# Kernel tuning notes

Hardware: AMD Instinct MI355X
Metric: run time of the kernel (lower is better)

The kernel has to match this reference:

```python
import jax, jax.numpy as jnp
import numpy as np

B, S, D, H, HID = 4, 1024, 1024, 16, 4096
DK = D // H
EPS = 1e-6


def _ln(x):
    # LayerNorm without affine, eps=1e-6
    mu = jnp.mean(x, axis=-1, keepdims=True)
    var = jnp.var(x, axis=-1, keepdims=True)
    return (x - mu) / jnp.sqrt(var + EPS)


def _lin(x, W, b):
    # torch Linear convention: W is [out, in]
    y = jnp.einsum('...i,oi->...o', x, W)
    return y + b if b is not None else y


def setup_inputs() -> dict:
    key = jax.random.key(0)
    ks = jax.random.split(key, 16)
    sc = lambda fan_in: 1.0 / np.sqrt(fan_in)
    inp = {
        'x': jax.random.normal(ks[0], (B, S, D), jnp.float32),
        'cond': jax.random.normal(ks[1], (B, 1, D), jnp.float32),
        'Wq': jax.random.normal(ks[2], (D, D), jnp.float32) * sc(D),
        'bq': jnp.zeros((D,), jnp.float32),
        'Wk': jax.random.normal(ks[3], (D, D), jnp.float32) * sc(D),
        'bk': jnp.zeros((D,), jnp.float32),
        'Wv': jax.random.normal(ks[4], (D, D), jnp.float32) * sc(D),
        'bv': jnp.zeros((D,), jnp.float32),
        'Wo': jax.random.normal(ks[5], (D, D), jnp.float32) * sc(D),
        'bo': jnp.zeros((D,), jnp.float32),
        'W1': jax.random.normal(ks[6], (HID, D), jnp.float32) * sc(D),
        'b1': jnp.zeros((HID,), jnp.float32),
        'W2': jax.random.normal(ks[7], (D, HID), jnp.float32) * sc(HID),
        'b2': jnp.zeros((D,), jnp.float32),
        'Wada': jax.random.normal(ks[8], (6 * D, D), jnp.float32) * sc(D),
        'bada': jnp.zeros((6 * D,), jnp.float32),
    }
    return inp


def reference(x, cond, Wq, bq, Wk, bk, Wv, bv, Wo, bo, W1, b1, W2, b2, Wada, bada):
    # adaLN modulation: SiLU -> Linear -> chunk 6 along last dim
    mod = _lin(jax.nn.silu(cond), Wada, bada)  # [B,1,6D]
    gama1, beta1, alpha1, gama2, beta2, alpha2 = jnp.split(mod, 6, axis=-1)

    # attention branch
    residual = x
    h = _ln(x) * (1.0 + beta1) + gama1  # modulate(shift=gama1, scale=beta1)
    q = _lin(h, Wq, bq).reshape(B, S, H, DK)
    k = _lin(h, Wk, bk).reshape(B, S, H, DK)
    v = _lin(h, Wv, bv).reshape(B, S, H, DK)
    scores = jnp.einsum('bqhd,bkhd->bhqk', q, k) / jnp.sqrt(jnp.float32(DK))
    probs = jax.nn.softmax(scores, axis=-1)
    attn = jnp.einsum('bhqk,bkhd->bqhd', probs, v).reshape(B, S, D)
    attn = _lin(attn, Wo, bo)
    x = residual + alpha1 * attn

    # MLP branch
    residual = x
    h = _ln(x) * (1.0 + beta2) + gama2
    h = _lin(h, W1, b1)
    h = jax.nn.gelu(h, approximate=False)  # torch nn.GELU default (erf)
    h = _lin(h, W2, b2)
    return residual + alpha2 * h
```

## Files before the change

### kernel.cpp

```cpp
#include <hip/hip_runtime.h>
#include <cstdint>

typedef __bf16 bf16_t;
typedef __bf16 bf16x4 __attribute__((ext_vector_type(4)));
typedef __bf16 bf16x8 __attribute__((ext_vector_type(8)));
typedef float f32x4 __attribute__((ext_vector_type(4)));

#define B_ 4
#define S_ 1024
#define D_ 1024
#define HID_ 4096
#define MEG (1u << 20)

static const size_t OFF_WBF  = 0;
static const size_t OFF_BQKV = 25165824;
static const size_t OFF_MOD  = 25178112;
static const size_t OFF_H    = 25276416;
static const size_t OFF_QKV  = 33665024;
static const size_t OFF_VT   = 58830848;
static const size_t OFF_ATTN = 67219456;
static const size_t OFF_X1   = 75608064;
static const size_t OFF_PART = 92385280;
static const size_t OFF_MLPH = 159494144;

__device__ __forceinline__ void async_copy16(const bf16_t* g, bf16_t* l) {
  __builtin_amdgcn_global_load_lds(
      (__attribute__((address_space(1))) void*)(g),
      (__attribute__((address_space(3))) void*)(l), 16, 0, 0);
}

__global__ __launch_bounds__(256) void convert_pack(
    const float* __restrict__ Wq, const float* __restrict__ Wk,
    const float* __restrict__ Wv, const float* __restrict__ Wo,
    const float* __restrict__ W1, const float* __restrict__ W2,
    const float* __restrict__ bq, const float* __restrict__ bk,
    const float* __restrict__ bv, bf16_t* __restrict__ wbf,
    float* __restrict__ bqkv) {
  const int y = blockIdx.y;
  if (y == 6) {
    int i = blockIdx.x * 256 + threadIdx.x;
    if (i < 3072)
      bqkv[i] = i < 1024 ? bq[i] : (i < 2048 ? bk[i - 1024] : bv[i - 2048]);
    return;
  }
  const float* src; bf16_t* dst; int n;
  switch (y) {
    case 0: src = Wq; dst = wbf;           n = MEG;     break;
    case 1: src = Wk; dst = wbf + MEG;     n = MEG;     break;
    case 2: src = Wv; dst = wbf + 2*MEG;   n = MEG;     break;
    case 3: src = Wo; dst = wbf + 3*MEG;   n = MEG;     break;
    case 4: src = W1; dst = wbf + 4*MEG;   n = 4*MEG;   break;
    default: src = W2; dst = wbf + 8*MEG;  n = 4*MEG;   break;
  }
  int idx = (blockIdx.x * 256 + threadIdx.x) * 4;
  if (idx < n) {
    float4 v = *(const float4*)(src + idx);
    bf16x4 pk;
    pk.x = (__bf16)v.x; pk.y = (__bf16)v.y; pk.z = (__bf16)v.z; pk.w = (__bf16)v.w;
    *(bf16x4*)(dst + idx) = pk;
  }
}

__global__ __launch_bounds__(256) void ada_mod(
    const float* __restrict__ cond, const float* __restrict__ Wada,
    const float* __restrict__ bada, float* __restrict__ mod) {
  const int wave = threadIdx.x >> 6, lane = threadIdx.x & 63;
  const int o = blockIdx.x * 4 + wave;
  const float* wr = Wada + (size_t)o * D_;
  float a0 = 0.f, a1 = 0.f, a2 = 0.f, a3 = 0.f;
#pragma unroll
  for (int l = 0; l < 16; l++) {
    int i = l * 64 + lane;
    float w = wr[i];
    float c0 = cond[i], c1 = cond[1024 + i], c2 = cond[2048 + i], c3 = cond[3072 + i];
    a0 += w * (c0 / (1.0f + __expf(-c0)));
    a1 += w * (c1 / (1.0f + __expf(-c1)));
    a2 += w * (c2 / (1.0f + __expf(-c2)));
    a3 += w * (c3 / (1.0f + __expf(-c3)));
  }
#pragma unroll
  for (int offs = 32; offs; offs >>= 1) {
    a0 += __shfl_xor(a0, offs);
    a1 += __shfl_xor(a1, offs);
    a2 += __shfl_xor(a2, offs);
    a3 += __shfl_xor(a3, offs);
  }
  if (lane == 0) {
    float bb = bada[o];
    mod[o]          = a0 + bb;
    mod[6144 + o]   = a1 + bb;
    mod[12288 + o]  = a2 + bb;
    mod[18432 + o]  = a3 + bb;
  }
}

__global__ __launch_bounds__(256) void ln_modulate(
    const float* __restrict__ X, const float* __restrict__ mod,
    bf16_t* __restrict__ H, int goff) {
  const int row = blockIdx.x;
  const int b = row >> 10;
  const int t = threadIdx.x;
  const float* xr = X + (size_t)row * D_;
  float4 xv = *(const float4*)(xr + t * 4);
  float s = xv.x + xv.y + xv.z + xv.w;
  float q = xv.x*xv.x + xv.y*xv.y + xv.z*xv.z + xv.w*xv.w;
  const int wave = t >> 6, lane = t & 63;
#pragma unroll
  for (int offs = 32; offs; offs >>= 1) {
    s += __shfl_down(s, offs);
    q += __shfl_down(q, offs);
  }
  __shared__ float sb[4][2];
  if (lane == 0) { sb[wave][0] = s; sb[wave][1] = q; }
  __syncthreads();
  float st = sb[0][0] + sb[1][0] + sb[2][0] + sb[3][0];
  float qt = sb[0][1] + sb[1][1] + sb[2][1] + sb[3][1];
  float mu = st * (1.0f / D_);
  float var = qt * (1.0f / D_) - mu * mu;
  float rstd = rsqrtf(var + 1e-6f);
  const float* mb = mod + (size_t)b * 6144 + goff;
  const int c = t * 4;
  float4 gm = *(const float4*)(mb + c);
  float4 bt = *(const float4*)(mb + 1024 + c);
  bf16x4 pk;
  pk.x = (__bf16)((xv.x - mu) * rstd * (1.0f + bt.x) + gm.x);
  pk.y = (__bf16)((xv.y - mu) * rstd * (1.0f + bt.y) + gm.y);
  pk.z = (__bf16)((xv.z - mu) * rstd * (1.0f + bt.z) + gm.z);
  pk.w = (__bf16)((xv.w - mu) * rstd * (1.0f + bt.w) + gm.w);
  *(bf16x4*)(H + (size_t)row * D_ + c) = pk;
}

__global__ __launch_bounds__(256) void transpose_v(
    const bf16_t* __restrict__ qkv, bf16_t* __restrict__ vT) {
  __shared__ bf16_t tile[64][65];
  const int bh = blockIdx.y;
  const int b = bh >> 4, hh = bh & 15;
  const int s0 = blockIdx.x * 64;
  const int t = threadIdx.x;
  const int tx = t & 63, ty = t >> 6;
  const bf16_t* src = qkv + (size_t)b * S_ * 3072 + 2048 + hh * 64;
  for (int r = ty; r < 64; r += 4)
    tile[r][tx] = src[(size_t)(s0 + r) * 3072 + tx];
  __syncthreads();
  bf16_t* dst = vT + (size_t)bh * 64 * 1024;
  for (int r = ty; r < 64; r += 4)
    dst[(size_t)r * 1024 + s0 + tx] = tile[tx][r];
}

__global__ __launch_bounds__(512, 4) void flash_attn(
    const bf16_t* __restrict__ qkv, const bf16_t* __restrict__ vT,
    bf16_t* __restrict__ attn) {
  __shared__ __align__(16) bf16_t Ks[2][2][64 * 64];
  __shared__ __align__(16) bf16_t Vs[2][2][64 * 64];
  __shared__ __align__(16) bf16_t Ps[8][16 * 64];

  const int t = threadIdx.x;
  const int wave = t >> 6, lane = t & 63;
  const int lm = lane & 15, quad = lane >> 4;
  const int bh = blockIdx.y;
  const int b = bh >> 4, hh = bh & 15;
  const int s0 = blockIdx.x * 128;

  const bf16_t* qbase = qkv + (size_t)b * S_ * 3072 + hh * 64;
  const bf16_t* kbase = qbase + 1024;
  const bf16_t* vbase = vT + (size_t)bh * (64 * 1024);

  const int row0 = t >> 3;
  const int cg = (t & 7) ^ (row0 & 7);
  const int od = t * 8;

  async_copy16(qbase + (size_t)(s0 + row0) * 3072 + cg * 8, &Ks[1][0][od]);
  async_copy16(qbase + (size_t)(s0 + 64 + row0) * 3072 + cg * 8, &Ks[1][1][od]);
  async_copy16(kbase + (size_t)row0 * 3072 + cg * 8, &Ks[0][0][od]);
  async_copy16(kbase + (size_t)(64 + row0) * 3072 + cg * 8, &Ks[0][1][od]);
  async_copy16(vbase + (size_t)row0 * 1024 + cg * 8, &Vs[0][0][od]);
  async_copy16(vbase + (size_t)row0 * 1024 + 64 + cg * 8, &Vs[0][1][od]);
  __syncthreads();

  bf16x8 aq0, aq1;
  {
    const int rq = wave * 16 + lm;
    const int qh = rq >> 6, qr = rq & 63;
    const int rbq = lm & 7;
    aq0 = *(const bf16x8*)&Ks[1][qh][qr * 64 + (quad ^ rbq) * 8];
    aq1 = *(const bf16x8*)&Ks[1][qh][qr * 64 + ((4 + quad) ^ rbq) * 8];
  }
  __syncthreads();

  f32x4 accO[4] = {};
  float mrow[4], lsum[4];
#pragma unroll
  for (int r = 0; r < 4; r++) { mrow[r] = -1e30f; lsum[r] = 0.f; }

  const float SC = 0.18033688f;
  const int rb = lm & 7;
  bf16_t* Pw = Ps[wave];

  for (int tt = 0; tt < 8; ++tt) {
    const int cur = tt & 1;
    if (tt < 7) {
      const int nb = cur ^ 1;
      const size_t k0n = (size_t)(tt + 1) << 7;
      async_copy16(kbase + (k0n + row0) * 3072 + cg * 8, &Ks[nb][0][od]);
      async_copy16(kbase + (k0n + 64 + row0) * 3072 + cg * 8, &Ks[nb][1][od]);
      async_copy16(vbase + (size_t)row0 * 1024 + k0n + cg * 8, &Vs[nb][0][od]);
      async_copy16(vbase + (size_t)row0 * 1024 + k0n + 64 + cg * 8, &Vs[nb][1][od]);
    }

    f32x4 accS[8];
#pragma unroll
    for (int j = 0; j < 8; j++) accS[j] = (f32x4){0.f, 0.f, 0.f, 0.f};
    __builtin_amdgcn_s_setprio(1);
#pragma unroll
    for (int hf = 0; hf < 2; hf++) {
#pragma unroll
      for (int ni = 0; ni < 4; ni++) {
        const int rk = ni * 16 + lm;
        bf16x8 b0 = *(const bf16x8*)&Ks[cur][hf][rk * 64 + ((quad ^ rb)) * 8];
        bf16x8 b1 = *(const bf16x8*)&Ks[cur][hf][rk * 64 + (((4 + quad) ^ rb)) * 8];
        f32x4 a = accS[hf * 4 + ni];
        a = __builtin_amdgcn_mfma_f32_16x16x32_bf16(aq0, b0, a, 0, 0, 0);
        a = __builtin_amdgcn_mfma_f32_16x16x32_bf16(aq1, b1, a, 0, 0, 0);
        accS[hf * 4 + ni] = a;
      }
    }
    __builtin_amdgcn_s_setprio(0);

    float mx[4];
#pragma unroll
    for (int r = 0; r < 4; r++) {
      float m0 = fmaxf(fmaxf(accS[0][r], accS[1][r]), fmaxf(accS[2][r], accS[3][r]));
      float m1 = fmaxf(fmaxf(accS[4][r], accS[5][r]), fmaxf(accS[6][r], accS[7][r]));
      float m8 = fmaxf(m0, m1);
      m8 = fmaxf(m8, __shfl_xor(m8, 1));
      m8 = fmaxf(m8, __shfl_xor(m8, 2));
      m8 = fmaxf(m8, __shfl_xor(m8, 4));
      m8 = fmaxf(m8, __shfl_xor(m8, 8));
      mx[r] = m8 * SC;
    }
    bool ok = (mx[0] - mrow[0] <= 8.0f) && (mx[1] - mrow[1] <= 8.0f) &&
              (mx[2] - mrow[2] <= 8.0f) && (mx[3] - mrow[3] <= 8.0f);
    if (!__all(ok)) {
#pragma unroll
      for (int r = 0; r < 4; r++) {
        float mnew = fmaxf(mrow[r], mx[r]);
        float al = exp2f(mrow[r] - mnew);
        mrow[r] = mnew;
        lsum[r] *= al;
#pragma unroll
        for (int di = 0; di < 4; di++) accO[di][r] *= al;
      }
    }
#pragma unroll
    for (int r = 0; r < 4; r++) {
      float sum = 0.f;
#pragma unroll
      for (int j = 0; j < 8; j++) {
        float p = exp2f(accS[j][r] * SC - mrow[r]);
        accS[j][r] = p;
        sum += p;
      }
      lsum[r] += sum;
    }

#pragma unroll
    for (int hf = 0; hf < 2; hf++) {
#pragma unroll
      for (int jj = 0; jj < 4; jj++)
#pragma unroll
        for (int r = 0; r < 4; r++) {
          int prow = quad * 4 + r;
          int c = jj * 16 + lm;
          Pw[prow * 64 + (((c >> 3) ^ (prow & 7)) << 3) + (c & 7)] =
              (__bf16)accS[hf * 4 + jj][r];
        }
      __builtin_amdgcn_s_setprio(1);
#pragma unroll
      for (int loc = 0; loc < 2; loc++) {
        bf16x8 ap = *(const bf16x8*)&Pw[lm * 64 + (((loc * 4 + quad) ^ rb)) * 8];
#pragma unroll
        for (int di = 0; di < 4; di++) {
          const int rv = di * 16 + lm;
          bf16x8 vv = *(const bf16x8*)&Vs[cur][hf]
              [rv * 64 + (((loc * 4 + quad) ^ rb)) * 8];
          accO[di] = __builtin_amdgcn_mfma_f32_16x16x32_bf16(ap, vv, accO[di], 0, 0, 0);
        }
      }
      __builtin_amdgcn_s_setprio(0);
    }
    __syncthreads();
  }

#pragma unroll
  for (int r = 0; r < 4; r++) {
    float sv = lsum[r];
    sv += __shfl_xor(sv, 1);
    sv += __shfl_xor(sv, 2);
    sv += __shfl_xor(sv, 4);
    sv += __shfl_xor(sv, 8);
    lsum[r] = sv;
  }

#pragma unroll
  for (int r = 0; r < 4; r++) {
    float inv = 1.0f / lsum[r];
    int prow = quad * 4 + r;
#pragma unroll
    for (int di = 0; di < 4; di++) {
      int col = di * 16 + lm;
      int cph = (col >> 3) ^ (prow & 7);
      Pw[prow * 64 + cph * 8 + (col & 7)] = (__bf16)(accO[di][r] * inv);
    }
  }
  bf16_t* abase = attn + (size_t)b * S_ * 1024 +
                  (size_t)(s0 + wave * 16) * 1024 + hh * 64;
#pragma unroll
  for (int it = 0; it < 2; it++) {
    int slot = it * 64 + lane;
    int orow = slot >> 3;
    int gc = slot & 7;
    int cph = gc ^ (orow & 7);
    bf16x8 val = *(const bf16x8*)&Pw[orow * 64 + cph * 8];
    *(bf16x8*)(abase + (size_t)orow * 1024 + gc * 8) = val;
  }
}

template <int EPI>
__global__ __launch_bounds__(512) void gemm_bt_big(
    const bf16_t* __restrict__ A, int lda,
    const bf16_t* __restrict__ B, int ldb,
    bf16_t* __restrict__ C, int ldc,
    int M, int N, int K,
    const float* __restrict__ bias) {
  __shared__ __align__(16) bf16_t As[2][4][64 * 64];
  __shared__ __align__(16) bf16_t Bs[2][4][64 * 64];

  const int gx = gridDim.x;
  int d = blockIdx.x + gx * blockIdx.y;
  const int cpx = (gx * gridDim.y) >> 3;
  int wg = (d & 7) * cpx + (d >> 3);
  const int by = wg / gx;
  const int bx = wg % gx;

  const int t = threadIdx.x;
  const int wave = t >> 6;
  const int lane = t & 63;
  const int lm = lane & 15;
  const int quad = lane >> 4;
  const int wr = wave >> 2;
  const int wc = wave & 3;

  const int m0 = by * 256;
  const int n0 = bx * 256;

  f32x4 acc[8][4] = {};

  const int srow = t >> 3;
  const int scg = (t & 7) ^ (srow & 7);
  const int sod = t * 8;
  const bf16_t* Ag = A + (size_t)(m0 + srow) * lda + scg * 8;
  const bf16_t* Bg = B + (size_t)(n0 + srow) * ldb + scg * 8;
  const size_t aStep = (size_t)64 * lda;
  const size_t bStep = (size_t)64 * ldb;

#define STAGE8(buf, ko)                                        \
  async_copy16(Ag + (ko), &As[buf][0][sod]);                   \
  async_copy16(Ag + aStep + (ko), &As[buf][1][sod]);           \
  async_copy16(Ag + 2 * aStep + (ko), &As[buf][2][sod]);       \
  async_copy16(Ag + 3 * aStep + (ko), &As[buf][3][sod]);       \
  async_copy16(Bg + (ko), &Bs[buf][0][sod]);                   \
  async_copy16(Bg + bStep + (ko), &Bs[buf][1][sod]);           \
  async_copy16(Bg + 2 * bStep + (ko), &Bs[buf][2][sod]);       \
  async_copy16(Bg + 3 * bStep + (ko), &Bs[buf][3][sod]);

  const int niter = K >> 6;
  STAGE8(0, 0);
  STAGE8(1, 64);

  const int rbx = lm & 7;
  const int sl0 = (quad ^ rbx) * 8;
  const int sl1 = ((4 + quad) ^ rbx) * 8;
  const int abase = wr * 8192 + lm * 64;
  const int bbase = wc * 4096 + lm * 64;

  int cur = 0;
  for (int it = 0; it < niter; ++it) {
    if (it + 1 < niter) {
      asm volatile("s_waitcnt vmcnt(8)" ::: "memory");
    } else {
      asm volatile("s_waitcnt vmcnt(0)" ::: "memory");
    }
    __builtin_amdgcn_s_barrier();

    const bf16_t* Ac = &As[cur][0][0];
    const bf16_t* Bc = &Bs[cur][0][0];

    bf16x8 afr[8][2], bfr[4][2];
#pragma unroll
    for (int mi = 0; mi < 8; mi++) {
      const int aoff = abase + (mi >> 2) * 4096 + (mi & 3) * 1024;
      afr[mi][0] = *(const bf16x8*)&Ac[aoff + sl0];
      afr[mi][1] = *(const bf16x8*)&Ac[aoff + sl1];
    }
#pragma unroll
    for (int ni = 0; ni < 4; ni++) {
      bfr[ni][0] = *(const bf16x8*)&Bc[bbase + ni * 1024 + sl0];
      bfr[ni][1] = *(const bf16x8*)&Bc[bbase + ni * 1024 + sl1];
    }
    asm volatile("s_waitcnt lgkmcnt(0)" ::: "memory");
    __builtin_amdgcn_sched_barrier(0);
    __builtin_amdgcn_s_barrier();

    if (it + 2 < niter) {
      const int ko = (it + 2) << 6;
      STAGE8(cur, ko);
    }

    __builtin_amdgcn_s_setprio(1);
#pragma unroll
    for (int mi = 0; mi < 8; mi++)
#pragma unroll
      for (int ni = 0; ni < 4; ni++) {
        acc[mi][ni] = __builtin_amdgcn_mfma_f32_16x16x32_bf16(
            afr[mi][0], bfr[ni][0], acc[mi][ni], 0, 0, 0);
        acc[mi][ni] = __builtin_amdgcn_mfma_f32_16x16x32_bf16(
            afr[mi][1], bfr[ni][1], acc[mi][ni], 0, 0, 0);
      }
    __builtin_amdgcn_s_setprio(0);
    cur ^= 1;
  }
#undef STAGE8

#pragma unroll
  for (int mi = 0; mi < 8; mi++) {
#pragma unroll
    for (int ni = 0; ni < 4; ni++) {
#pragma unroll
      for (int r = 0; r < 4; r++) {
        int row = m0 + wr * 128 + mi * 16 + quad * 4 + r;
        int col = n0 + wc * 64 + ni * 16 + lm;
        float v = acc[mi][ni][r];
        size_t idx = (size_t)row * ldc + col;
        if (EPI == 0) {
          if (bias) v += bias[col];
          C[idx] = (__bf16)v;
        } else if (EPI == 3) {
          v += bias[col];
          float u = 1.5957691216f * (v + 0.044715f * v * v * v);
          float g = v / (1.0f + __expf(-u));
          C[idx] = (__bf16)g;
        }
      }
    }
  }
}

template <int EPI>
__global__ __launch_bounds__(512) void gemm_bt(
    const bf16_t* __restrict__ A, int lda, long long sAz,
    const bf16_t* __restrict__ B, int ldb, long long sBz,
    void* __restrict__ Cv, int ldc, long long sCz,
    int M, int N, int K,
    const float* __restrict__ bias,
    float scale) {
  __shared__ __align__(16) bf16_t As[3][256 * 64];
  __shared__ __align__(16) bf16_t Bs[3][128 * 64];

  const int z = blockIdx.z;
  A += (size_t)z * sAz;
  B += (size_t)z * sBz;

  const int gx = gridDim.x;
  int d = blockIdx.x + gx * blockIdx.y;
  {
    const int cpx = (gx * gridDim.y) >> 3;
    int wg = (d & 7) * cpx + (d >> 3);
    const int by = wg / gx;
    const int bx = wg % gx;

    const int t = threadIdx.x;
    const int wave = t >> 6;
    const int lane = t & 63;
    const int lm = lane & 15;
    const int quad = lane >> 4;
    const int wr = wave >> 1;
    const int wc = wave & 1;

    const int m0 = by * 256;
    const int n0 = bx * 128;

    f32x4 acc[4][4] = {};

    const int srow = t >> 3;
    const int scg = (t & 7) ^ (srow & 7);
    const int sod = t * 8;
    const bf16_t* Ag = A + (size_t)(m0 + srow) * lda + scg * 8;
    const bf16_t* Bg = B + (size_t)(n0 + srow) * ldb + scg * 8;
    const size_t a64 = (size_t)64 * lda, a128 = (size_t)128 * lda,
                 a192 = (size_t)192 * lda, b64 = (size_t)64 * ldb;

#define STAGE6(buf, ko)                                      \
  async_copy16(Ag + (ko), &As[buf][sod]);                    \
  async_copy16(Ag + a64 + (ko), &As[buf][4096 + sod]);       \
  async_copy16(Ag + a128 + (ko), &As[buf][8192 + sod]);      \
  async_copy16(Ag + a192 + (ko), &As[buf][12288 + sod]);     \
  async_copy16(Bg + (ko), &Bs[buf][sod]);                    \
  async_copy16(Bg + b64 + (ko), &Bs[buf][4096 + sod]);

    const int niter = K >> 6;
    STAGE6(0, 0);
    STAGE6(1, 64);

    const int rbx = lm & 7;
    const int sl0 = (quad ^ rbx) * 8;
    const int sl1 = ((4 + quad) ^ rbx) * 8;
    const int arow = wr * 4096 + lm * 64;
    const int brow = wc * 4096 + lm * 64;

    int cur = 0;
    for (int it = 0; it < niter; ++it) {
      if (it + 1 < niter) {
        asm volatile("s_waitcnt vmcnt(6)" ::: "memory");
      } else {
        asm volatile("s_waitcnt vmcnt(0)" ::: "memory");
      }
      __builtin_amdgcn_s_barrier();
      const int nb = (cur >= 1) ? cur - 1 : 2;
      const int ko = (it + 2) << 6;
      const bool st = (it + 2 < niter);

      bf16x8 af0[2], af1[2], bfr[4][2];
      af0[0] = *(const bf16x8*)&As[cur][arow + sl0];
      af0[1] = *(const bf16x8*)&As[cur][arow + sl1];
      af1[0] = *(const bf16x8*)&As[cur][arow + 1024 + sl0];
      af1[1] = *(const bf16x8*)&As[cur][arow + 1024 + sl1];
#pragma unroll
      for (int i = 0; i < 4; i++) {
        bfr[i][0] = *(const bf16x8*)&Bs[cur][brow + i * 1024 + sl0];
        bfr[i][1] = *(const bf16x8*)&Bs[cur][brow + i * 1024 + sl1];
      }
      if (st) {
        async_copy16(Ag + ko, &As[nb][sod]);
        async_copy16(Ag + a64 + ko, &As[nb][4096 + sod]);
        async_copy16(Ag + a128 + ko, &As[nb][8192 + sod]);
      }
      __builtin_amdgcn_s_barrier();
      __builtin_amdgcn_s_setprio(1);
#pragma unroll
      for (int ks = 0; ks < 2; ks++)
#pragma unroll
        for (int ni = 0; ni < 4; ni++) {
          acc[0][ni] = __builtin_amdgcn_mfma_f32_16x16x32_bf16(
              af0[ks], bfr[ni][ks], acc[0][ni], 0, 0, 0);
          acc[1][ni] = __builtin_amdgcn_mfma_f32_16x16x32_bf16(
              af1[ks], bfr[ni][ks], acc[1][ni], 0, 0, 0);
        }
      __builtin_amdgcn_s_setprio(0);
      __builtin_amdgcn_s_barrier();

      bf16x8 af2[2], af3[2];
      af2[0] = *(const bf16x8*)&As[cur][arow + 2048 + sl0];
      af2[1] = *(const bf16x8*)&As[cur][arow + 2048 + sl1];
      af3[0] = *(const bf16x8*)&As[cur][arow + 3072 + sl0];
      af3[1] = *(const bf16x8*)&As[cur][arow + 3072 + sl1];
      if (st) {
        async_copy16(Ag + a192 + ko, &As[nb][12288 + sod]);
        async_copy16(Bg + ko, &Bs[nb][sod]);
        async_copy16(Bg + b64 + ko, &Bs[nb][4096 + sod]);
      }
      __builtin_amdgcn_s_barrier();
      __builtin_amdgcn_s_setprio(1);
#pragma unroll
      for (int ks = 0; ks < 2; ks++)
#pragma unroll
        for (int ni = 0; ni < 4; ni++) {
          acc[2][ni] = __builtin_amdgcn_mfma_f32_16x16x32_bf16(
              af2[ks], bfr[ni][ks], acc[2][ni], 0, 0, 0);
          acc[3][ni] = __builtin_amdgcn_mfma_f32_16x16x32_bf16(
              af3[ks], bfr[ni][ks], acc[3][ni], 0, 0, 0);
        }
      __builtin_amdgcn_s_setprio(0);
      cur = (cur == 2) ? 0 : cur + 1;
    }
#undef STAGE6

    const size_t cz = (size_t)z * sCz;
#pragma unroll
    for (int mi = 0; mi < 4; mi++) {
#pragma unroll
      for (int ni = 0; ni < 4; ni++) {
#pragma unroll
        for (int r = 0; r < 4; r++) {
          int row = m0 + wr * 64 + mi * 16 + quad * 4 + r;
          int col = n0 + wc * 64 + ni * 16 + lm;
          float v = acc[mi][ni][r];
          size_t idx = cz + (size_t)row * ldc + col;
          if (EPI == 1) {
            ((float*)Cv)[idx] = v * scale;
          } else if (EPI == 0) {
            if (bias) v += bias[col];
            ((bf16_t*)Cv)[idx] = (__bf16)v;
          } else if (EPI == 3) {
            v += bias[col];
            float u = 1.5957691216f * (v + 0.044715f * v * v * v);
            float g = v / (1.0f + __expf(-u));
            ((bf16_t*)Cv)[idx] = (__bf16)g;
          }
        }
      }
    }
  }
}

__global__ __launch_bounds__(256) void reduce_ln(
    const float* __restrict__ part, const float* __restrict__ x,
    const float* __restrict__ bo, const float* __restrict__ mod,
    float* __restrict__ x1, bf16_t* __restrict__ h) {
  const int row = blockIdx.x;
  const int b = row >> 10;
  const int t = threadIdx.x;
  const int c = t * 4;
  const size_t idx = (size_t)row * 1024 + c;
  float4 p0 = *(const float4*)(part + idx);
  float4 p1 = *(const float4*)(part + 4194304 + idx);
  float4 bb = *(const float4*)(bo + c);
  float4 al = *(const float4*)(mod + (size_t)b * 6144 + 2048 + c);
  float4 xs = *(const float4*)(x + idx);
  float4 xv;
  xv.x = xs.x + al.x * (p0.x + p1.x + bb.x);
  xv.y = xs.y + al.y * (p0.y + p1.y + bb.y);
  xv.z = xs.z + al.z * (p0.z + p1.z + bb.z);
  xv.w = xs.w + al.w * (p0.w + p1.w + bb.w);
  *(float4*)(x1 + idx) = xv;

  float s = xv.x + xv.y + xv.z + xv.w;
  float q = xv.x*xv.x + xv.y*xv.y + xv.z*xv.z + xv.w*xv.w;
  const int wave = t >> 6, lane = t & 63;
#pragma unroll
  for (int offs = 32; offs; offs >>= 1) {
    s += __shfl_down(s, offs);
    q += __shfl_down(q, offs);
  }
  __shared__ float sb[4][2];
  if (lane == 0) { sb[wave][0] = s; sb[wave][1] = q; }
  __syncthreads();
  float st = sb[0][0] + sb[1][0] + sb[2][0] + sb[3][0];
  float qt = sb[0][1] + sb[1][1] + sb[2][1] + sb[3][1];
  float mu = st * (1.0f / D_);
  float var = qt * (1.0f / D_) - mu * mu;
  float rstd = rsqrtf(var + 1e-6f);
  const float* mb = mod + (size_t)b * 6144 + 3072;
  float4 gm = *(const float4*)(mb + c);
  float4 bt = *(const float4*)(mb + 1024 + c);
  bf16x4 pk;
  pk.x = (__bf16)((xv.x - mu) * rstd * (1.0f + bt.x) + gm.x);
  pk.y = (__bf16)((xv.y - mu) * rstd * (1.0f + bt.y) + gm.y);
  pk.z = (__bf16)((xv.z - mu) * rstd * (1.0f + bt.z) + gm.z);
  pk.w = (__bf16)((xv.w - mu) * rstd * (1.0f + bt.w) + gm.w);
  *(bf16x4*)(h + idx) = pk;
}

__global__ __launch_bounds__(256) void reduce_w2(
    const float* __restrict__ part, const float* __restrict__ x1,
    const float* __restrict__ b2, const float* __restrict__ mod,
    float* __restrict__ out) {
  const int idx = (blockIdx.x * 256 + threadIdx.x) * 4;
  const int col = idx & 1023;
  const int row = idx >> 10;
  const int b = row >> 10;
  float4 s0 = *(const float4*)(part + idx);
  float4 s1 = *(const float4*)(part + 4194304 + idx);
  float4 bb = *(const float4*)(b2 + col);
  float4 al = *(const float4*)(mod + (size_t)b * 6144 + 5120 + col);
  float4 rs = *(const float4*)(x1 + idx);
  float4 o;
  o.x = rs.x + al.x * (s0.x + s1.x + bb.x);
  o.y = rs.y + al.y * (s0.y + s1.y + bb.y);
  o.z = rs.z + al.z * (s0.z + s1.z + bb.z);
  o.w = rs.w + al.w * (s0.w + s1.w + bb.w);
  *(float4*)(out + idx) = o;
}

extern "C" void kernel_launch(void* const* d_in, const int* in_sizes, int n_in,
                              void* d_out, int out_size, void* d_ws, size_t ws_size,
                              hipStream_t stream) {
  (void)in_sizes; (void)n_in; (void)out_size; (void)ws_size;
  const float* x    = (const float*)d_in[0];
  const float* cond = (const float*)d_in[1];
  const float* Wq   = (const float*)d_in[2];
  const float* bq   = (const float*)d_in[3];
  const float* Wk   = (const float*)d_in[4];
  const float* bk   = (const float*)d_in[5];
  const float* Wv   = (const float*)d_in[6];
  const float* bv   = (const float*)d_in[7];
  const float* Wo   = (const float*)d_in[8];
  const float* bo   = (const float*)d_in[9];
  const float* W1   = (const float*)d_in[10];
  const float* b1   = (const float*)d_in[11];
  const float* W2   = (const float*)d_in[12];
  const float* b2   = (const float*)d_in[13];
  const float* Wada = (const float*)d_in[14];
  const float* bada = (const float*)d_in[15];

  uint8_t* ws = (uint8_t*)d_ws;
  bf16_t* wbf   = (bf16_t*)(ws + OFF_WBF);
  float*  bqkv  = (float*)(ws + OFF_BQKV);
  float*  mod   = (float*)(ws + OFF_MOD);
  bf16_t* h     = (bf16_t*)(ws + OFF_H);
  bf16_t* qkv   = (bf16_t*)(ws + OFF_QKV);
  bf16_t* vT    = (bf16_t*)(ws + OFF_VT);
  bf16_t* attn  = (bf16_t*)(ws + OFF_ATTN);
  float*  x1    = (float*)(ws + OFF_X1);
  float*  part  = (float*)(ws + OFF_PART);
  bf16_t* mlph  = (bf16_t*)(ws + OFF_MLPH);
  float* out = (float*)d_out;

  convert_pack<<<dim3(4096, 7, 1), 256, 0, stream>>>(Wq, Wk, Wv, Wo, W1, W2,
                                                     bq, bk, bv, wbf, bqkv);
  ada_mod<<<1536, 256, 0, stream>>>(cond, Wada, bada, mod);
  ln_modulate<<<4096, 256, 0, stream>>>(x, mod, h, 0);
  gemm_bt_big<0><<<dim3(12, 16, 1), 512, 0, stream>>>(
      h, 1024, wbf, 1024, qkv, 3072, 4096, 3072, 1024, bqkv);
  transpose_v<<<dim3(16, 64, 1), 256, 0, stream>>>(qkv, vT);
  flash_attn<<<dim3(8, 64, 1), 512, 0, stream>>>(qkv, vT, attn);

  gemm_bt<1><<<dim3(8, 16, 2), 512, 0, stream>>>(
      attn, 1024, 512, wbf + (size_t)3 * MEG, 1024, 512, part, 1024, 4194304,
      4096, 1024, 512, nullptr, 1.f);
  reduce_ln<<<4096, 256, 0, stream>>>(part, x, bo, mod, x1, h);

  gemm_bt_big<3><<<dim3(16, 16, 1), 512, 0, stream>>>(
      h, 1024, wbf + (size_t)4 * MEG, 1024, mlph, 4096, 4096, 4096, 1024, b1);
  gemm_bt<1><<<dim3(8, 16, 2), 512, 0, stream>>>(
      mlph, 4096, 2048, wbf + (size_t)8 * MEG, 4096, 2048, part, 1024, 4194304,
      4096, 1024, 2048, nullptr, 1.f);
  reduce_w2<<<4096, 256, 0, stream>>>(part, x1, b2, mod, out);
}
```

Measured before the change: 378.3 us.

## Use 256x256 tile split-K GEMM for Wo/W2 and swizzle flash-attn blocks

Replaces the 256x128 triple-buffered split-K=2 GEMM used for the Wo and W2 projections with a 256x256-tile, double-buffered kernel using split-K=4, keeping the grid at 256 blocks while raising arithmetic intensity per tile. The reduce kernels now sum four fp32 partials instead of two, which adds memory traffic. Flash attention block indices are remapped so consecutive blocks cover different heads, aiming to spread L2/K-V reuse across the dies. The larger tile uses 32 accumulators per wave, which raises register pressure and limits occupancy.

```diff
diff --git a/kernel.cpp b/kernel.cpp
--- a/kernel.cpp
+++ b/kernel.cpp
@@ -157,9 +157,10 @@
   const int t = threadIdx.x;
   const int wave = t >> 6, lane = t & 63;
   const int lm = lane & 15, quad = lane >> 4;
-  const int bh = blockIdx.y;
+  const int d = blockIdx.x + 8 * blockIdx.y;
+  const int bh = ((d & 7) << 3) + ((d >> 3) & 7);
   const int b = bh >> 4, hh = bh & 15;
-  const int s0 = blockIdx.x * 128;
+  const int s0 = (d >> 6) * 128;
 
   const bf16_t* qbase = qkv + (size_t)b * S_ * 3072 + hh * 64;
   const bf16_t* kbase = qbase + 1024;
@@ -455,158 +456,124 @@
   }
 }
 
-template <int EPI>
-__global__ __launch_bounds__(512) void gemm_bt(
+__global__ __launch_bounds__(512) void gemm_bt_big_s(
     const bf16_t* __restrict__ A, int lda, long long sAz,
     const bf16_t* __restrict__ B, int ldb, long long sBz,
-    void* __restrict__ Cv, int ldc, long long sCz,
-    int M, int N, int K,
-    const float* __restrict__ bias,
-    float scale) {
-  __shared__ __align__(16) bf16_t As[3][256 * 64];
-  __shared__ __align__(16) bf16_t Bs[3][128 * 64];
+    float* __restrict__ C, int ldc, long long sCz,
+    int M, int N, int K) {
+  __shared__ __align__(16) bf16_t As[2][4][64 * 64];
+  __shared__ __align__(16) bf16_t Bs[2][4][64 * 64];
 
   const int z = blockIdx.z;
   A += (size_t)z * sAz;
   B += (size_t)z * sBz;
+  C += (size_t)z * sCz;
 
   const int gx = gridDim.x;
   int d = blockIdx.x + gx * blockIdx.y;
-  {
-    const int cpx = (gx * gridDim.y) >> 3;
-    int wg = (d & 7) * cpx + (d >> 3);
-    const int by = wg / gx;
-    const int bx = wg % gx;
-
-    const int t = threadIdx.x;
-    const int wave = t >> 6;
-    const int lane = t & 63;
-    const int lm = lane & 15;
-    const int quad = lane >> 4;
-    const int wr = wave >> 1;
-    const int wc = wave & 1;
-
-    const int m0 = by * 256;
-    const int n0 = bx * 128;
-
-    f32x4 acc[4][4] = {};
-
-    const int srow = t >> 3;
-    const int scg = (t & 7) ^ (srow & 7);
-    const int sod = t * 8;
-    const bf16_t* Ag = A + (size_t)(m0 + srow) * lda + scg * 8;
-    const bf16_t* Bg = B + (size_t)(n0 + srow) * ldb + scg * 8;
-    const size_t a64 = (size_t)64 * lda, a128 = (size_t)128 * lda,
-                 a192 = (size_t)192 * lda, b64 = (size_t)64 * ldb;
-
-#define STAGE6(buf, ko)                                      \
-  async_copy16(Ag + (ko), &As[buf][sod]);                    \
-  async_copy16(Ag + a64 + (ko), &As[buf][4096 + sod]);       \
-  async_copy16(Ag + a128 + (ko), &As[buf][8192 + sod]);      \
-  async_copy16(Ag + a192 + (ko), &As[buf][12288 + sod]);     \
-  async_copy16(Bg + (ko), &Bs[buf][sod]);                    \
-  async_copy16(Bg + b64 + (ko), &Bs[buf][4096 + sod]);
-
-    const int niter = K >> 6;
-    STAGE6(0, 0);
-    STAGE6(1, 64);
-
-    const int rbx = lm & 7;
-    const int sl0 = (quad ^ rbx) * 8;
-    const int sl1 = ((4 + quad) ^ rbx) * 8;
-    const int arow = wr * 4096 + lm * 64;
-    const int brow = wc * 4096 + lm * 64;
-
-    int cur = 0;
-    for (int it = 0; it < niter; ++it) {
-      if (it + 1 < niter) {
-        asm volatile("s_waitcnt vmcnt(6)" ::: "memory");
-      } else {
-        asm volatile("s_waitcnt vmcnt(0)" ::: "memory");
+  const int cpx = (gx * gridDim.y) >> 3;
+  int wg = (d & 7) * cpx + (d >> 3);
+  const int by = wg / gx;
+  const int bx = wg % gx;
+
+  const int t = threadIdx.x;
+  const int wave = t >> 6;
+  const int lane = t & 63;
+  const int lm = lane & 15;
+  const int quad = lane >> 4;
+  const int wr = wave >> 2;
+  const int wc = wave & 3;
+
+  const int m0 = by * 256;
+  const int n0 = bx * 256;
+
+  f32x4 acc[8][4] = {};
+
+  const int srow = t >> 3;
+  const int scg = (t & 7) ^ (srow & 7);
+  const int sod = t * 8;
+  const bf16_t* Ag = A + (size_t)(m0 + srow) * lda + scg * 8;
+  const bf16_t* Bg = B + (size_t)(n0 + srow) * ldb + scg * 8;
+  const size_t aStep = (size_t)64 * lda;
+  const size_t bStep = (size_t)64 * ldb;
+
+#define STAGE8(buf, ko)                                        \
+  async_copy16(Ag + (ko), &As[buf][0][sod]);                   \
+  async_copy16(Ag + aStep + (ko), &As[buf][1][sod]);           \
+  async_copy16(Ag + 2 * aStep + (ko), &As[buf][2][sod]);       \
+  async_copy16(Ag + 3 * aStep + (ko), &As[buf][3][sod]);       \
+  async_copy16(Bg + (ko), &Bs[buf][0][sod]);                   \
+  async_copy16(Bg + bStep + (ko), &Bs[buf][1][sod]);           \
+  async_copy16(Bg + 2 * bStep + (ko), &Bs[buf][2][sod]);       \
+  async_copy16(Bg + 3 * bStep + (ko), &Bs[buf][3][sod]);
+
+  const int niter = K >> 6;
+  STAGE8(0, 0);
+  STAGE8(1, 64);
+
+  const int rbx = lm & 7;
+  const int sl0 = (quad ^ rbx) * 8;
+  const int sl1 = ((4 + quad) ^ rbx) * 8;
+  const int abase = wr * 8192 + lm * 64;
+  const int bbase = wc * 4096 + lm * 64;
+
+  int cur = 0;
+  for (int it = 0; it < niter; ++it) {
+    if (it + 1 < niter) {
+      asm volatile("s_waitcnt vmcnt(8)" ::: "memory");
+    } else {
+      asm volatile("s_waitcnt vmcnt(0)" ::: "memory");
+    }
+    __builtin_amdgcn_s_barrier();
+
+    const bf16_t* Ac = &As[cur][0][0];
+    const bf16_t* Bc = &Bs[cur][0][0];
+
+    bf16x8 afr[8][2], bfr[4][2];
+#pragma unroll
+    for (int mi = 0; mi < 8; mi++) {
+      const int aoff = abase + (mi >> 2) * 4096 + (mi & 3) * 1024;
+      afr[mi][0] = *(const bf16x8*)&Ac[aoff + sl0];
+      afr[mi][1] = *(const bf16x8*)&Ac[aoff + sl1];
+    }
+#pragma unroll
+    for (int ni = 0; ni < 4; ni++) {
+      bfr[ni][0] = *(const bf16x8*)&Bc[bbase + ni * 1024 + sl0];
+      bfr[ni][1] = *(const bf16x8*)&Bc[bbase + ni * 1024 + sl1];
+    }
+    asm volatile("s_waitcnt lgkmcnt(0)" ::: "memory");
+    __builtin_amdgcn_sched_barrier(0);
+    __builtin_amdgcn_s_barrier();
+
+    if (it + 2 < niter) {
+      const int ko = (it + 2) << 6;
+      STAGE8(cur, ko);
+    }
+
+    __builtin_amdgcn_s_setprio(1);
+#pragma unroll
+    for (int mi = 0; mi < 8; mi++)
+#pragma unroll
+      for (int ni = 0; ni < 4; ni++) {
+        acc[mi][ni] = __builtin_amdgcn_mfma_f32_16x16x32_bf16(
+            afr[mi][0], bfr[ni][0], acc[mi][ni], 0, 0, 0);
+        acc[mi][ni] = __builtin_amdgcn_mfma_f32_16x16x32_bf16(
+            afr[mi][1], bfr[ni][1], acc[mi][ni], 0, 0, 0);
       }
-      __builtin_amdgcn_s_barrier();
-      const int nb = (cur >= 1) ? cur - 1 : 2;
-      const int ko = (it + 2) << 6;
-      const bool st = (it + 2 < niter);
-
-      bf16x8 af0[2], af1[2], bfr[4][2];
-      af0[0] = *(const bf16x8*)&As[cur][arow + sl0];
-      af0[1] = *(const bf16x8*)&As[cur][arow + sl1];
-      af1[0] = *(const bf16x8*)&As[cur][arow + 1024 + sl0];
-      af1[1] = *(const bf16x8*)&As[cur][arow + 1024 + sl1];
-#pragma unroll
-      for (int i = 0; i < 4; i++) {
-        bfr[i][0] = *(const bf16x8*)&Bs[cur][brow + i * 1024 + sl0];
-        bfr[i][1] = *(const bf16x8*)&Bs[cur][brow + i * 1024 + sl1];
-      }
-      if (st) {
-        async_copy16(Ag + ko, &As[nb][sod]);
-        async_copy16(Ag + a64 + ko, &As[nb][4096 + sod]);
-        async_copy16(Ag + a128 + ko, &As[nb][8192 + sod]);
-      }
-      __builtin_amdgcn_s_barrier();
-      __builtin_amdgcn_s_setprio(1);
-#pragma unroll
-      for (int ks = 0; ks < 2; ks++)
-#pragma unroll
-        for (int ni = 0; ni < 4; ni++) {
-          acc[0][ni] = __builtin_amdgcn_mfma_f32_16x16x32_bf16(
-              af0[ks], bfr[ni][ks], acc[0][ni], 0, 0, 0);
-          acc[1][ni] = __builtin_amdgcn_mfma_f32_16x16x32_bf16(
-              af1[ks], bfr[ni][ks], acc[1][ni], 0, 0, 0);
-        }
-      __builtin_amdgcn_s_setprio(0);
-      __builtin_amdgcn_s_barrier();
-
-      bf16x8 af2[2], af3[2];
-      af2[0] = *(const bf16x8*)&As[cur][arow + 2048 + sl0];
-      af2[1] = *(const bf16x8*)&As[cur][arow + 2048 + sl1];
-      af3[0] = *(const bf16x8*)&As[cur][arow + 3072 + sl0];
-      af3[1] = *(const bf16x8*)&As[cur][arow + 3072 + sl1];
-      if (st) {
-        async_copy16(Ag + a192 + ko, &As[nb][12288 + sod]);
-        async_copy16(Bg + ko, &Bs[nb][sod]);
-        async_copy16(Bg + b64 + ko, &Bs[nb][4096 + sod]);
-      }
-      __builtin_amdgcn_s_barrier();
-      __builtin_amdgcn_s_setprio(1);
-#pragma unroll
-      for (int ks = 0; ks < 2; ks++)
-#pragma unroll
-        for (int ni = 0; ni < 4; ni++) {
-          acc[2][ni] = __builtin_amdgcn_mfma_f32_16x16x32_bf16(
-              af2[ks], bfr[ni][ks], acc[2][ni], 0, 0, 0);
-          acc[3][ni] = __builtin_amdgcn_mfma_f32_16x16x32_bf16(
-              af3[ks], bfr[ni][ks], acc[3][ni], 0, 0, 0);
-        }
-      __builtin_amdgcn_s_setprio(0);
-      cur = (cur == 2) ? 0 : cur + 1;
-    }
-#undef STAGE6
-
-    const size_t cz = (size_t)z * sCz;
-#pragma unroll
-    for (int mi = 0; mi < 4; mi++) {
-#pragma unroll
-      for (int ni = 0; ni < 4; ni++) {
-#pragma unroll
-        for (int r = 0; r < 4; r++) {
-          int row = m0 + wr * 64 + mi * 16 + quad * 4 + r;
-          int col = n0 + wc * 64 + ni * 16 + lm;
-          float v = acc[mi][ni][r];
-          size_t idx = cz + (size_t)row * ldc + col;
-          if (EPI == 1) {
-            ((float*)Cv)[idx] = v * scale;
-          } else if (EPI == 0) {
-            if (bias) v += bias[col];
-            ((bf16_t*)Cv)[idx] = (__bf16)v;
-          } else if (EPI == 3) {
-            v += bias[col];
-            float u = 1.5957691216f * (v + 0.044715f * v * v * v);
-            float g = v / (1.0f + __expf(-u));
-            ((bf16_t*)Cv)[idx] = (__bf16)g;
-          }
-        }
+    __builtin_amdgcn_s_setprio(0);
+    cur ^= 1;
+  }
+#undef STAGE8
+
+#pragma unroll
+  for (int mi = 0; mi < 8; mi++) {
+#pragma unroll
+    for (int ni = 0; ni < 4; ni++) {
+#pragma unroll
+      for (int r = 0; r < 4; r++) {
+        int row = m0 + wr * 128 + mi * 16 + quad * 4 + r;
+        int col = n0 + wc * 64 + ni * 16 + lm;
+        C[(size_t)row * ldc + col] = acc[mi][ni][r];
       }
     }
   }
@@ -623,14 +590,16 @@
   const size_t idx = (size_t)row * 1024 + c;
   float4 p0 = *(const float4*)(part + idx);
   float4 p1 = *(const float4*)(part + 4194304 + idx);
+  float4 p2 = *(const float4*)(part + 8388608 + idx);
+  float4 p3 = *(const float4*)(part + 12582912 + idx);
   float4 bb = *(const float4*)(bo + c);
   float4 al = *(const float4*)(mod + (size_t)b * 6144 + 2048 + c);
   float4 xs = *(const float4*)(x + idx);
   float4 xv;
-  xv.x = xs.x + al.x * (p0.x + p1.x + bb.x);
-  xv.y = xs.y + al.y * (p0.y + p1.y + bb.y);
-  xv.z = xs.z + al.z * (p0.z + p1.z + bb.z);
-  xv.w = xs.w + al.w * (p0.w + p1.w + bb.w);
+  xv.x = xs.x + al.x * (p0.x + p1.x + p2.x + p3.x + bb.x);
+  xv.y = xs.y + al.y * (p0.y + p1.y + p2.y + p3.y + bb.y);
+  xv.z = xs.z + al.z * (p0.z + p1.z + p2.z + p3.z + bb.z);
+  xv.w = xs.w + al.w * (p0.w + p1.w + p2.w + p3.w + bb.w);
   *(float4*)(x1 + idx) = xv;
 
   float s = xv.x + xv.y + xv.z + xv.w;
@@ -670,14 +639,16 @@
   const int b = row >> 10;
   float4 s0 = *(const float4*)(part + idx);
   float4 s1 = *(const float4*)(part + 4194304 + idx);
+  float4 s2 = *(const float4*)(part + 8388608 + idx);
+  float4 s3 = *(const float4*)(part + 12582912 + idx);
   float4 bb = *(const float4*)(b2 + col);
   float4 al = *(const float4*)(mod + (size_t)b * 6144 + 5120 + col);
   float4 rs = *(const float4*)(x1 + idx);
   float4 o;
-  o.x = rs.x + al.x * (s0.x + s1.x + bb.x);
-  o.y = rs.y + al.y * (s0.y + s1.y + bb.y);
-  o.z = rs.z + al.z * (s0.z + s1.z + bb.z);
-  o.w = rs.w + al.w * (s0.w + s1.w + bb.w);
+  o.x = rs.x + al.x * (s0.x + s1.x + s2.x + s3.x + bb.x);
+  o.y = rs.y + al.y * (s0.y + s1.y + s2.y + s3.y + bb.y);
+  o.z = rs.z + al.z * (s0.z + s1.z + s2.z + s3.z + bb.z);
+  o.w = rs.w + al.w * (s0.w + s1.w + s2.w + s3.w + bb.w);
   *(float4*)(out + idx) = o;
 }
 
@@ -724,15 +695,15 @@
   transpose_v<<<dim3(16, 64, 1), 256, 0, stream>>>(qkv, vT);
   flash_attn<<<dim3(8, 64, 1), 512, 0, stream>>>(qkv, vT, attn);
 
-  gemm_bt<1><<<dim3(8, 16, 2), 512, 0, stream>>>(
-      attn, 1024, 512, wbf + (size_t)3 * MEG, 1024, 512, part, 1024, 4194304,
-      4096, 1024, 512, nullptr, 1.f);
+  gemm_bt_big_s<<<dim3(4, 16, 4), 512, 0, stream>>>(
+      attn, 1024, 256, wbf + (size_t)3 * MEG, 1024, 256, part, 1024, 4194304,
+      4096, 1024, 256);
   reduce_ln<<<4096, 256, 0, stream>>>(part, x, bo, mod, x1, h);
 
   gemm_bt_big<3><<<dim3(16, 16, 1), 512, 0, stream>>>(
       h, 1024, wbf + (size_t)4 * MEG, 1024, mlph, 4096, 4096, 4096, 1024, b1);
-  gemm_bt<1><<<dim3(8, 16, 2), 512, 0, stream>>>(
-      mlph, 4096, 2048, wbf + (size_t)8 * MEG, 4096, 2048, part, 1024, 4194304,
-      4096, 1024, 2048, nullptr, 1.f);
+  gemm_bt_big_s<<<dim3(4, 16, 4), 512, 0, stream>>>(
+      mlph, 4096, 1024, wbf + (size_t)8 * MEG, 4096, 1024, part, 1024, 4194304,
+      4096, 1024, 1024);
   reduce_w2<<<4096, 256, 0, stream>>>(part, x1, b2, mod, out);
 }
```

New measurement: 385.7 us. About the same (+2.0%).
